# Kernel optimization log

Hardware: AMD Instinct MI355X
Metric: run time of the kernel (lower is better)

The kernel has to match this reference:

```python
import jax, jax.numpy as jnp
import numpy as np

NUM_CLS = 81
N_ROI = 512
N_POS = 128
OUT = 7
SAMP = 2
SCALES = (0.25, 0.125, 0.0625, 0.03125)


def _roi_align(feat, rois, out, scale, samp=SAMP):
    # feat: [C,H,W]; rois: [N,4] (x1,y1,x2,y2) in image coords. torchvision-style
    # ROIAlign, aligned=False, avg pool over samp x samp bilinear samples per bin.
    C, H, W = feat.shape
    b = rois * scale
    x1, y1, x2, y2 = b[:, 0], b[:, 1], b[:, 2], b[:, 3]
    bw = jnp.maximum(x2 - x1, 1.0) / out
    bh = jnp.maximum(y2 - y1, 1.0) / out
    N = rois.shape[0]
    # sample offsets within a roi, in bin units: [out, samp]
    grid = jnp.arange(out, dtype=feat.dtype)[:, None] + (jnp.arange(samp, dtype=feat.dtype)[None, :] + 0.5) / samp
    px = x1[:, None, None] + grid[None] * bw[:, None, None]  # [N,out,samp]
    py = y1[:, None, None] + grid[None] * bh[:, None, None]
    # full sampling grid [N, out_y, out_x, samp_y, samp_x]
    PX = jnp.broadcast_to(px[:, None, :, None, :], (N, out, out, samp, samp))
    PY = jnp.broadcast_to(py[:, :, None, :, None], (N, out, out, samp, samp))
    valid = (PX > -1.0) & (PX < W) & (PY > -1.0) & (PY < H)
    x = jnp.clip(PX, 0.0, W - 1.0)
    y = jnp.clip(PY, 0.0, H - 1.0)
    x0f = jnp.floor(x)
    y0f = jnp.floor(y)
    lx = x - x0f
    ly = y - y0f
    x0 = x0f.astype(jnp.int32)
    y0 = y0f.astype(jnp.int32)
    x1i = jnp.minimum(x0 + 1, W - 1)
    y1i = jnp.minimum(y0 + 1, H - 1)
    def g(yi, xi):
        return feat[:, yi, xi]  # [C,N,out,out,samp,samp]
    v = (g(y0, x0) * (1 - ly) * (1 - lx) + g(y0, x1i) * (1 - ly) * lx
         + g(y1i, x0) * ly * (1 - lx) + g(y1i, x1i) * ly * lx)
    v = v * valid.astype(feat.dtype)
    pooled = v.mean(axis=(-1, -2))  # [C,N,out,out]
    return pooled.transpose(1, 0, 2, 3)  # [N,C,out,out]


def setup_inputs() -> dict:
    key = jax.random.key(0)
    ks = jax.random.split(key, 16)
    H_IMG, W_IMG = 800.0, 1024.0
    P2 = jax.random.normal(ks[0], (1, 256, 200, 256), jnp.float32)
    P3 = jax.random.normal(ks[1], (1, 256, 100, 128), jnp.float32)
    P4 = jax.random.normal(ks[2], (1, 256, 50, 64), jnp.float32)
    P5 = jax.random.normal(ks[3], (1, 256, 25, 32), jnp.float32)
    x1 = jax.random.uniform(ks[4], (N_ROI,)) * (W_IMG - 64.0)
    y1 = jax.random.uniform(ks[5], (N_ROI,)) * (H_IMG - 64.0)
    w = jax.random.uniform(ks[6], (N_ROI,), minval=16.0, maxval=512.0)
    h = jax.random.uniform(ks[7], (N_ROI,), minval=16.0, maxval=512.0)
    rois = jnp.stack([x1, y1, jnp.minimum(x1 + w, W_IMG - 1.0), jnp.minimum(y1 + h, H_IMG - 1.0)], axis=-1)
    label = jax.random.randint(ks[8], (N_ROI,), 0, NUM_CLS, dtype=jnp.int32)
    loc = jax.random.normal(ks[9], (N_POS, 4), jnp.float32) * 0.1
    s = 0.02
    return {
        'P2': P2, 'P3': P3, 'P4': P4, 'P5': P5,
        'rois': rois, 'label': label, 'loc': loc,
        'W1': jax.random.normal(ks[10], (256 * OUT * OUT, 1024), jnp.float32) * s,
        'b1': jnp.zeros((1024,), jnp.float32),
        'W2': jax.random.normal(ks[11], (1024, 1024), jnp.float32) * s,
        'b2': jnp.zeros((1024,), jnp.float32),
        'Wcls': jax.random.normal(ks[12], (1024, NUM_CLS), jnp.float32) * s,
        'bcls': jnp.zeros((NUM_CLS,), jnp.float32),
        'Wloc': jax.random.normal(ks[13], (1024, NUM_CLS * 4), jnp.float32) * s,
        'bloc': jnp.zeros((NUM_CLS * 4,), jnp.float32),
    }


def reference(P2, P3, P4, P5, rois, label, loc, W1, b1, W2, b2, Wcls, bcls, Wloc, bloc):
    feats = (P2[0], P3[0], P4[0], P5[0])
    # FPN level assignment: floor(4 + log2(sqrt(area)/224)).clamp(2,5) - 2
    area = (rois[:, 2] - rois[:, 0] + 1.0) * (rois[:, 3] - rois[:, 1] + 1.0)
    lvl = jnp.floor(4.0 + jnp.log(jnp.sqrt(area) / 224.0) / np.log(2.0))
    lvl = (jnp.clip(lvl, 2.0, 5.0) - 2.0).astype(jnp.int32)  # [N] in {0,1,2,3}
    onehot = jax.nn.one_hot(lvl, 4, dtype=rois.dtype)  # [N,4]
    # pool every roi at all 4 levels, select assigned level (same values as
    # the original per-level grouping + argsort re-ordering)
    pooled = jnp.stack([_roi_align(f, rois, OUT, s) for f, s in zip(feats, SCALES)])  # [4,N,C,7,7]
    x = jnp.einsum('lnchw,nl->nchw', pooled, onehot)
    # Fast head
    x = x.reshape(x.shape[0], -1)
    h = jax.nn.relu(x @ W1 + b1)
    h = jax.nn.relu(h @ W2 + b2)
    logits = h @ Wcls + bcls                    # [N, num_cls]
    locp = (h @ Wloc + bloc).reshape(-1, NUM_CLS, 4)
    # loss assembly
    logp = jax.nn.log_softmax(logits, axis=-1)
    cls_loss = -jnp.take_along_axis(logp, label[:, None], axis=1).mean()
    loc_train = locp[jnp.arange(N_POS), label[:N_POS]]  # class-indexed gather
    t = jnp.abs(loc_train - loc)
    sl1 = jnp.where(t < 1.0, 0.5 * t * t, t - 0.5)  # SmoothL1, sigma=1
    box_loss = sl1.sum() / float(N_ROI)
    return cls_loss + box_loss
```

## Files before the change

### kernel.cpp

```cpp
#include <hip/hip_runtime.h>
#include <hip/hip_bf16.h>
#include <math.h>

#define N_ROI 512
#define N_POS 128
#define NUM_CLS 81
#define KDIM 12544
#define HID 1024

typedef __bf16 bf16x8 __attribute__((ext_vector_type(8)));
typedef __bf16 bf16x4 __attribute__((ext_vector_type(4)));
typedef float f32x4 __attribute__((ext_vector_type(4)));

__device__ inline void gload16(const void* g, void* lds) {
  __builtin_amdgcn_global_load_lds(
      (const __attribute__((address_space(1))) void*)g,
      (__attribute__((address_space(3))) void*)lds, 16, 0, 0);
}

__global__ __launch_bounds__(256) void roi_align_kernel(
    const float* __restrict__ P2, const float* __restrict__ P3,
    const float* __restrict__ P4, const float* __restrict__ P5,
    const float* __restrict__ rois, __bf16* __restrict__ xout) {
  int n = blockIdx.x;
  int t = threadIdx.x;

  __shared__ int    gxo[14];
  __shared__ float2 gxf[14];
  __shared__ int2   gyi[14];
  __shared__ float2 gyf[14];
  __shared__ int    s_lvl, s_HWb;

  float rx1 = rois[n * 4 + 0], ry1 = rois[n * 4 + 1];
  float rx2 = rois[n * 4 + 2], ry2 = rois[n * 4 + 3];
  float area = (rx2 - rx1 + 1.0f) * (ry2 - ry1 + 1.0f);
  float lf = floorf(4.0f + log2f(sqrtf(area) / 224.0f));
  lf = fminf(fmaxf(lf, 2.0f), 5.0f);
  int lvl = (int)lf - 2;

  const float scales[4] = {0.25f, 0.125f, 0.0625f, 0.03125f};
  const int   Hs[4] = {200, 100, 50, 25};
  const int   Ws[4] = {256, 128, 64, 32};
  float sc = scales[lvl];
  int H = Hs[lvl], W = Ws[lvl];

  float bx1 = rx1 * sc, by1 = ry1 * sc;
  float bw = fmaxf(rx2 * sc - bx1, 1.0f) * (1.0f / 7.0f);
  float bh = fmaxf(ry2 * sc - by1, 1.0f) * (1.0f / 7.0f);

  if (t < 14) {
    int i = t >> 1, j = t & 1;
    float g = (float)i + 0.25f + 0.5f * (float)j;
    float px = bx1 + g * bw;
    float vx = (px > -1.0f && px < (float)W) ? 1.0f : 0.0f;
    float xx = fminf(fmaxf(px, 0.0f), (float)(W - 1));
    float x0f = floorf(xx);
    int x0 = (int)x0f;
    int xa = min(x0, W - 2);
    float lxp = (x0 > xa) ? 1.0f : (xx - x0f);
    gxo[t] = xa * 4;
    gxf[t] = make_float2(lxp, vx);
    if (t == 0) { s_lvl = lvl; s_HWb = H * W * 4; }
  } else if (t >= 64 && t < 78) {
    int s = t - 64;
    int i = s >> 1, j = s & 1;
    float g = (float)i + 0.25f + 0.5f * (float)j;
    float py = by1 + g * bh;
    float vy = (py > -1.0f && py < (float)H) ? 1.0f : 0.0f;
    float yy = fminf(fmaxf(py, 0.0f), (float)(H - 1));
    float y0f = floorf(yy);
    int y0 = (int)y0f;
    int y1 = min(y0 + 1, H - 1);
    gyi[s] = make_int2(y0 * W * 4, y1 * W * 4);
    gyf[s] = make_float2(yy - y0f, vy);
  }
  __syncthreads();

  int lvl_s = __builtin_amdgcn_readfirstlane(s_lvl);
  const char* base = (const char*)(lvl_s == 0 ? P2 : lvl_s == 1 ? P3
                                   : lvl_s == 2 ? P4 : P5);
  int HWb = s_HWb;

  int wave = t >> 6, lane = t & 63;
  if (lane >= 49) return;

  int oh = (lane * 37) >> 8;
  int ow = lane - oh * 7;

  int2   xo = *(const int2*)&gxo[2 * ow];
  float4 xf = *(const float4*)&gxf[2 * ow];
  int4   yi = *(const int4*)&gyi[2 * oh];
  float4 yf = *(const float4*)&gyf[2 * oh];

  int off[8];
  off[0] = yi.x + xo.x; off[1] = yi.y + xo.x;
  off[2] = yi.x + xo.y; off[3] = yi.y + xo.y;
  off[4] = yi.z + xo.x; off[5] = yi.w + xo.x;
  off[6] = yi.z + xo.y; off[7] = yi.w + xo.y;

  float w00 = yf.y * xf.y, w01 = yf.y * xf.w;
  float w10 = yf.w * xf.y, w11 = yf.w * xf.w;

  int c0 = blockIdx.y * 16 + wave * 4;
  const char* bc0 = base + (size_t)c0 * HWb;

  float2 g[4][8];
#pragma unroll
  for (int ch = 0; ch < 4; ++ch) {
    const char* bcc = bc0 + (size_t)ch * HWb;
#pragma unroll
    for (int l = 0; l < 8; ++l)
      g[ch][l] = *(const float2*)(bcc + off[l]);
  }

  __bf16* outp = xout + (size_t)n * KDIM + (size_t)c0 * 49 + lane;
#pragma unroll
  for (int ch = 0; ch < 4; ++ch) {
    float s = 0.0f;
    {
      float fa = g[ch][0].x + xf.x * (g[ch][0].y - g[ch][0].x);
      float fb = g[ch][1].x + xf.x * (g[ch][1].y - g[ch][1].x);
      s += (fa + yf.x * (fb - fa)) * w00;
    }
    {
      float fa = g[ch][2].x + xf.z * (g[ch][2].y - g[ch][2].x);
      float fb = g[ch][3].x + xf.z * (g[ch][3].y - g[ch][3].x);
      s += (fa + yf.x * (fb - fa)) * w01;
    }
    {
      float fa = g[ch][4].x + xf.x * (g[ch][4].y - g[ch][4].x);
      float fb = g[ch][5].x + xf.x * (g[ch][5].y - g[ch][5].x);
      s += (fa + yf.z * (fb - fa)) * w10;
    }
    {
      float fa = g[ch][6].x + xf.z * (g[ch][6].y - g[ch][6].x);
      float fb = g[ch][7].x + xf.z * (g[ch][7].y - g[ch][7].x);
      s += (fa + yf.z * (fb - fa)) * w11;
    }
    outp[ch * 49] = (__bf16)(s * 0.25f);
  }
}

__global__ __launch_bounds__(256) void transpose_to_bf16_64(
    const float* __restrict__ src, __bf16* __restrict__ dst, int R, int C) {
  __shared__ float tile[64][65];
  int t = threadIdx.x;
  int bc = blockIdx.x * 64, br = blockIdx.y * 64;
  int rr = t >> 4, c4 = (t & 15) * 4;
#pragma unroll
  for (int p = 0; p < 4; ++p) {
    int r = p * 16 + rr;
    f32x4 v = *(const f32x4*)&src[(size_t)(br + r) * C + bc + c4];
    tile[r][c4] = v.x; tile[r][c4 + 1] = v.y;
    tile[r][c4 + 2] = v.z; tile[r][c4 + 3] = v.w;
  }
  __syncthreads();
#pragma unroll
  for (int p = 0; p < 2; ++p) {
    int group = t + 256 * p;
    int c = group >> 3;
    int r0 = (group & 7) * 8;
    bf16x8 o;
#pragma unroll
    for (int j = 0; j < 8; ++j) o[j] = (__bf16)tile[r0 + j][c];
    *(bf16x8*)&dst[(size_t)(bc + c) * R + br + r0] = o;
  }
}

__global__ __launch_bounds__(256) void transpose_pad_cls(
    const float* __restrict__ Wcls, __bf16* __restrict__ WcT) {
  __shared__ float tile[64][65];
  int t = threadIdx.x;
  int bk = blockIdx.x * 64;
  int bj = blockIdx.y * 64;
  int rr = t >> 4, c4 = (t & 15) * 4;
#pragma unroll
  for (int p = 0; p < 4; ++p) {
    int k = bk + p * 16 + rr;
#pragma unroll
    for (int i = 0; i < 4; ++i) {
      int j = bj + c4 + i;
      tile[p * 16 + rr][c4 + i] =
          (j < NUM_CLS) ? Wcls[(size_t)k * NUM_CLS + j] : 0.0f;
    }
  }
  __syncthreads();
#pragma unroll
  for (int p = 0; p < 4; ++p) {
    int c = p * 16 + rr;
    int r4 = c4;
    bf16x4 o = {(__bf16)tile[r4][c], (__bf16)tile[r4 + 1][c],
                (__bf16)tile[r4 + 2][c], (__bf16)tile[r4 + 3][c]};
    *(bf16x4*)&WcT[(size_t)(bj + c) * 1024 + bk + r4] = o;
  }
}

__global__ __launch_bounds__(256, 2) void mfma_gemm128(
    const __bf16* __restrict__ A, const __bf16* __restrict__ Bt,
    float* __restrict__ part, int M, int N, int K, int chunk) {
  __shared__ __align__(16) unsigned char smem[16384];
  unsigned char* As = smem;
  unsigned char* Bs = smem + 8192;

  int t = threadIdx.x;
  int wave = t >> 6;
  int lane = t & 63;
  int fr = lane & 15, q = lane >> 4;
  int bm = blockIdx.y * 128, bn = blockIdx.x * 128;
  int wm = (wave >> 1) * 64, wn = (wave & 1) * 64;

  int kbeg = blockIdx.z * chunk;
  int kend = min(K, kbeg + chunk);

  int qsrc = ((t & 3) - ((t >> 3) & 3)) & 3;
  const __bf16* a0 = A + (size_t)(bm + (t >> 2)) * K + kbeg + qsrc * 8;
  const __bf16* a1 = a0 + (size_t)64 * K;
  const __bf16* b0 = Bt + (size_t)(bn + (t >> 2)) * K + kbeg + qsrc * 8;
  const __bf16* b1 = b0 + (size_t)64 * K;
  unsigned char* AsW = As + wave * 1024;
  unsigned char* BsW = Bs + wave * 1024;

  int sA = ((q + (fr >> 1)) & 3) * 16;

  f32x4 acc[4][4];
#pragma unroll
  for (int i = 0; i < 4; ++i)
#pragma unroll
    for (int j = 0; j < 4; ++j) acc[i][j] = (f32x4){0.f, 0.f, 0.f, 0.f};

  for (int k0 = kbeg; k0 < kend; k0 += 32) {
    __syncthreads();
    gload16(a0, AsW);
    gload16(a1, AsW + 4096);
    gload16(b0, BsW);
    gload16(b1, BsW + 4096);
    a0 += 32; a1 += 32; b0 += 32; b1 += 32;
    __syncthreads();

    bf16x8 af[4], bfr[4];
#pragma unroll
    for (int i = 0; i < 4; ++i)
      af[i] = *(const bf16x8*)(As + (wm + 16 * i + fr) * 64 + sA);
#pragma unroll
    for (int j = 0; j < 4; ++j)
      bfr[j] = *(const bf16x8*)(Bs + (wn + 16 * j + fr) * 64 + sA);
#pragma unroll
    for (int i = 0; i < 4; ++i)
#pragma unroll
      for (int j = 0; j < 4; ++j)
        acc[i][j] = __builtin_amdgcn_mfma_f32_16x16x32_bf16(af[i], bfr[j],
                                                            acc[i][j], 0, 0, 0);
  }

  float* P = part + (size_t)blockIdx.z * M * N;
#pragma unroll
  for (int i = 0; i < 4; ++i) {
#pragma unroll
    for (int j = 0; j < 4; ++j) {
      int row0 = bm + wm + 16 * i + q * 4;
      int col = bn + wn + 16 * j + fr;
#pragma unroll
      for (int r = 0; r < 4; ++r)
        P[(size_t)(row0 + r) * N + col] = acc[i][j][r];
    }
  }
}

__global__ __launch_bounds__(256) void reduce_kernel(
    const float* __restrict__ part, int S, int MN, int Nmask,
    const float* __restrict__ bias, int bias_n, int relu,
    float* __restrict__ outf, __bf16* __restrict__ outb) {
  int i4 = (blockIdx.x * 256 + threadIdx.x) * 4;
  if (i4 >= MN) return;
  f32x4 s = {0.f, 0.f, 0.f, 0.f};
  for (int z = 0; z < S; ++z) {
    f32x4 v = *(const f32x4*)&part[(size_t)z * MN + i4];
    s.x += v.x; s.y += v.y; s.z += v.z; s.w += v.w;
  }
  int col = i4 & Nmask;
  float r[4] = {s.x, s.y, s.z, s.w};
#pragma unroll
  for (int j = 0; j < 4; ++j) {
    float b = (col + j < bias_n) ? bias[col + j] : 0.0f;
    float v = r[j] + b;
    if (relu) v = fmaxf(v, 0.0f);
    r[j] = v;
  }
  if (outf) {
    f32x4 o = {r[0], r[1], r[2], r[3]};
    *(f32x4*)&outf[i4] = o;
  }
  if (outb) {
    bf16x4 o = {(__bf16)r[0], (__bf16)r[1], (__bf16)r[2], (__bf16)r[3]};
    *(bf16x4*)&outb[i4] = o;
  }
}

__global__ __launch_bounds__(256) void loc_head_kernel(
    const float* __restrict__ h2, const float* __restrict__ Wloc,
    const float* __restrict__ bloc, const int* __restrict__ label,
    float* __restrict__ loct) {
  int n = blockIdx.x;
  int d = threadIdx.x >> 6;
  int lane = threadIdx.x & 63;
  int lab = label[n];
  const float* h = h2 + (size_t)n * HID;
  const float* w = Wloc + (size_t)lab * 4 + d;
  float s = 0.0f;
#pragma unroll
  for (int i = 0; i < 16; ++i) {
    int k = lane + i * 64;
    s += h[k] * w[(size_t)k * (NUM_CLS * 4)];
  }
#pragma unroll
  for (int off = 32; off > 0; off >>= 1) s += __shfl_down(s, off);
  if (lane == 0) loct[n * 4 + d] = s + bloc[lab * 4 + d];
}

__global__ __launch_bounds__(512) void loss_kernel(
    const float* __restrict__ logits, const int* __restrict__ label,
    const float* __restrict__ loct, const float* __restrict__ loc,
    float* __restrict__ out) {
  int t = threadIdx.x;
  const float* row = logits + (size_t)t * 128;
  float m = -1e30f;
  for (int j = 0; j < NUM_CLS; ++j) m = fmaxf(m, row[j]);
  float se = 0.0f;
  for (int j = 0; j < NUM_CLS; ++j) se += expf(row[j] - m);
  float cl = (m + logf(se)) - row[label[t]];

  float a = fabsf(loct[t] - loc[t]);
  float bl = (a < 1.0f) ? 0.5f * a * a : a - 0.5f;

  float v = cl + bl;
#pragma unroll
  for (int off = 32; off > 0; off >>= 1) v += __shfl_down(v, off);

  __shared__ float red[8];
  if ((t & 63) == 0) red[t >> 6] = v;
  __syncthreads();
  if (t == 0) {
    float tot = 0.0f;
    for (int i = 0; i < 8; ++i) tot += red[i];
    out[0] = tot * (1.0f / (float)N_ROI);
  }
}

extern "C" void kernel_launch(void* const* d_in, const int* in_sizes, int n_in,
                              void* d_out, int out_size, void* d_ws, size_t ws_size,
                              hipStream_t stream) {
  const float* P2   = (const float*)d_in[0];
  const float* P3   = (const float*)d_in[1];
  const float* P4   = (const float*)d_in[2];
  const float* P5   = (const float*)d_in[3];
  const float* rois = (const float*)d_in[4];
  const int*   label= (const int*)d_in[5];
  const float* loc  = (const float*)d_in[6];
  const float* W1   = (const float*)d_in[7];
  const float* b1   = (const float*)d_in[8];
  const float* W2   = (const float*)d_in[9];
  const float* b2   = (const float*)d_in[10];
  const float* Wcls = (const float*)d_in[11];
  const float* bcls = (const float*)d_in[12];
  const float* Wloc = (const float*)d_in[13];
  const float* bloc = (const float*)d_in[14];
  float* out = (float*)d_out;

  char* w = (char*)d_ws;
  __bf16* xb  = (__bf16*)w;  w += (size_t)N_ROI * KDIM * 2;
  __bf16* W1t = (__bf16*)w;  w += (size_t)KDIM * HID * 2;
  __bf16* W2t = (__bf16*)w;  w += (size_t)HID * HID * 2;
  __bf16* WcT = (__bf16*)w;  w += (size_t)128 * HID * 2;
  __bf16* h1b = (__bf16*)w;  w += (size_t)N_ROI * HID * 2;
  __bf16* h2b = (__bf16*)w;  w += (size_t)N_ROI * HID * 2;
  float*  h2f = (float*)w;   w += (size_t)N_ROI * HID * 4;
  float*  logits = (float*)w; w += (size_t)N_ROI * 128 * 4;
  float*  loct = (float*)w;  w += (size_t)N_ROI * 4;
  float*  part = (float*)w;

  transpose_to_bf16_64<<<dim3(HID / 64, KDIM / 64), 256, 0, stream>>>(W1, W1t,
                                                                      KDIM, HID);
  transpose_to_bf16_64<<<dim3(HID / 64, HID / 64), 256, 0, stream>>>(W2, W2t,
                                                                     HID, HID);
  transpose_pad_cls<<<dim3(16, 2), 256, 0, stream>>>(Wcls, WcT);
  roi_align_kernel<<<dim3(N_ROI, 16), 256, 0, stream>>>(P2, P3, P4, P5, rois,
                                                        xb);

  mfma_gemm128<<<dim3(HID / 128, N_ROI / 128, 16), 256, 0, stream>>>(
      xb, W1t, part, N_ROI, HID, KDIM, 800);
  reduce_kernel<<<(N_ROI * HID) / 1024, 256, 0, stream>>>(
      part, 16, N_ROI * HID, HID - 1, b1, HID, 1, nullptr, h1b);

  mfma_gemm128<<<dim3(HID / 128, N_ROI / 128, 8), 256, 0, stream>>>(
      h1b, W2t, part, N_ROI, HID, HID, 128);
  reduce_kernel<<<(N_ROI * HID) / 1024, 256, 0, stream>>>(
      part, 8, N_ROI * HID, HID - 1, b2, HID, 1, h2f, h2b);

  mfma_gemm128<<<dim3(1, N_ROI / 128, 4), 256, 0, stream>>>(
      h2b, WcT, part, N_ROI, 128, HID, 256);
  reduce_kernel<<<(N_ROI * 128) / 1024, 256, 0, stream>>>(
      part, 4, N_ROI * 128, 127, bcls, NUM_CLS, 0, logits, nullptr);

  loc_head_kernel<<<N_POS, 256, 0, stream>>>(h2f, Wloc, bloc, label, loct);
  loss_kernel<<<1, 512, 0, stream>>>(logits, label, loct, loc, out);
}
```

Baseline: 292.7 us.

## Fuse ROI-align and weight transposes into one prep kernel launch

Merges the ROI-align kernel and the three weight-transpose/convert kernels into a single launch that dispatches on block index, so independent work shares one grid and runs concurrently instead of as serial launches. Each ROI-align block now handles 8 channels per wave instead of 4, which raises register use. The class-head GEMM's split-K is doubled from 4 to 8, with a matching change to the reduce. The trade-off is higher register pressure in the fused kernel, tile shared memory that ROI blocks do not need, and more partial sums to reduce.

Result: faster. 284.9 us (-2.6%).

```diff
diff --git a/kernel.cpp b/kernel.cpp
--- a/kernel.cpp
+++ b/kernel.cpp
@@ -18,141 +18,168 @@
       (__attribute__((address_space(3))) void*)lds, 16, 0, 0);
 }
 
-__global__ __launch_bounds__(256) void roi_align_kernel(
+__global__ __launch_bounds__(256, 2) void prep_kernel(
     const float* __restrict__ P2, const float* __restrict__ P3,
     const float* __restrict__ P4, const float* __restrict__ P5,
-    const float* __restrict__ rois, __bf16* __restrict__ xout) {
-  int n = blockIdx.x;
-  int t = threadIdx.x;
-
+    const float* __restrict__ rois, __bf16* __restrict__ xout,
+    const float* __restrict__ W1, __bf16* __restrict__ W1t,
+    const float* __restrict__ W2, __bf16* __restrict__ W2t,
+    const float* __restrict__ Wcls, __bf16* __restrict__ WcT) {
+  __shared__ float tile[64][65];
   __shared__ int    gxo[14];
   __shared__ float2 gxf[14];
   __shared__ int2   gyi[14];
   __shared__ float2 gyf[14];
   __shared__ int    s_lvl, s_HWb;
 
-  float rx1 = rois[n * 4 + 0], ry1 = rois[n * 4 + 1];
-  float rx2 = rois[n * 4 + 2], ry2 = rois[n * 4 + 3];
-  float area = (rx2 - rx1 + 1.0f) * (ry2 - ry1 + 1.0f);
-  float lf = floorf(4.0f + log2f(sqrtf(area) / 224.0f));
-  lf = fminf(fmaxf(lf, 2.0f), 5.0f);
-  int lvl = (int)lf - 2;
-
-  const float scales[4] = {0.25f, 0.125f, 0.0625f, 0.03125f};
-  const int   Hs[4] = {200, 100, 50, 25};
-  const int   Ws[4] = {256, 128, 64, 32};
-  float sc = scales[lvl];
-  int H = Hs[lvl], W = Ws[lvl];
-
-  float bx1 = rx1 * sc, by1 = ry1 * sc;
-  float bw = fmaxf(rx2 * sc - bx1, 1.0f) * (1.0f / 7.0f);
-  float bh = fmaxf(ry2 * sc - by1, 1.0f) * (1.0f / 7.0f);
-
-  if (t < 14) {
-    int i = t >> 1, j = t & 1;
-    float g = (float)i + 0.25f + 0.5f * (float)j;
-    float px = bx1 + g * bw;
-    float vx = (px > -1.0f && px < (float)W) ? 1.0f : 0.0f;
-    float xx = fminf(fmaxf(px, 0.0f), (float)(W - 1));
-    float x0f = floorf(xx);
-    int x0 = (int)x0f;
-    int xa = min(x0, W - 2);
-    float lxp = (x0 > xa) ? 1.0f : (xx - x0f);
-    gxo[t] = xa * 4;
-    gxf[t] = make_float2(lxp, vx);
-    if (t == 0) { s_lvl = lvl; s_HWb = H * W * 4; }
-  } else if (t >= 64 && t < 78) {
-    int s = t - 64;
-    int i = s >> 1, j = s & 1;
-    float g = (float)i + 0.25f + 0.5f * (float)j;
-    float py = by1 + g * bh;
-    float vy = (py > -1.0f && py < (float)H) ? 1.0f : 0.0f;
-    float yy = fminf(fmaxf(py, 0.0f), (float)(H - 1));
-    float y0f = floorf(yy);
-    int y0 = (int)y0f;
-    int y1 = min(y0 + 1, H - 1);
-    gyi[s] = make_int2(y0 * W * 4, y1 * W * 4);
-    gyf[s] = make_float2(yy - y0f, vy);
-  }
-  __syncthreads();
-
-  int lvl_s = __builtin_amdgcn_readfirstlane(s_lvl);
-  const char* base = (const char*)(lvl_s == 0 ? P2 : lvl_s == 1 ? P3
-                                   : lvl_s == 2 ? P4 : P5);
-  int HWb = s_HWb;
-
-  int wave = t >> 6, lane = t & 63;
-  if (lane >= 49) return;
-
-  int oh = (lane * 37) >> 8;
-  int ow = lane - oh * 7;
-
-  int2   xo = *(const int2*)&gxo[2 * ow];
-  float4 xf = *(const float4*)&gxf[2 * ow];
-  int4   yi = *(const int4*)&gyi[2 * oh];
-  float4 yf = *(const float4*)&gyf[2 * oh];
-
-  int off[8];
-  off[0] = yi.x + xo.x; off[1] = yi.y + xo.x;
-  off[2] = yi.x + xo.y; off[3] = yi.y + xo.y;
-  off[4] = yi.z + xo.x; off[5] = yi.w + xo.x;
-  off[6] = yi.z + xo.y; off[7] = yi.w + xo.y;
-
-  float w00 = yf.y * xf.y, w01 = yf.y * xf.w;
-  float w10 = yf.w * xf.y, w11 = yf.w * xf.w;
-
-  int c0 = blockIdx.y * 16 + wave * 4;
-  const char* bc0 = base + (size_t)c0 * HWb;
-
-  float2 g[4][8];
-#pragma unroll
-  for (int ch = 0; ch < 4; ++ch) {
-    const char* bcc = bc0 + (size_t)ch * HWb;
-#pragma unroll
-    for (int l = 0; l < 8; ++l)
-      g[ch][l] = *(const float2*)(bcc + off[l]);
-  }
-
-  __bf16* outp = xout + (size_t)n * KDIM + (size_t)c0 * 49 + lane;
-#pragma unroll
-  for (int ch = 0; ch < 4; ++ch) {
-    float s = 0.0f;
-    {
-      float fa = g[ch][0].x + xf.x * (g[ch][0].y - g[ch][0].x);
-      float fb = g[ch][1].x + xf.x * (g[ch][1].y - g[ch][1].x);
+  int bid = blockIdx.x;
+  int t = threadIdx.x;
+
+  if (bid < 4096) {
+    int n = bid & 511;
+    int grp = bid >> 9;
+
+    float rx1 = rois[n * 4 + 0], ry1 = rois[n * 4 + 1];
+    float rx2 = rois[n * 4 + 2], ry2 = rois[n * 4 + 3];
+    float area = (rx2 - rx1 + 1.0f) * (ry2 - ry1 + 1.0f);
+    float lf = floorf(4.0f + log2f(sqrtf(area) / 224.0f));
+    lf = fminf(fmaxf(lf, 2.0f), 5.0f);
+    int lvl = (int)lf - 2;
+
+    const float scales[4] = {0.25f, 0.125f, 0.0625f, 0.03125f};
+    const int   Hs[4] = {200, 100, 50, 25};
+    const int   Ws[4] = {256, 128, 64, 32};
+    float sc = scales[lvl];
+    int H = Hs[lvl], W = Ws[lvl];
+
+    float bx1 = rx1 * sc, by1 = ry1 * sc;
+    float bw = fmaxf(rx2 * sc - bx1, 1.0f) * (1.0f / 7.0f);
+    float bh = fmaxf(ry2 * sc - by1, 1.0f) * (1.0f / 7.0f);
+
+    if (t < 14) {
+      int i = t >> 1, j = t & 1;
+      float g = (float)i + 0.25f + 0.5f * (float)j;
+      float px = bx1 + g * bw;
+      float vx = (px > -1.0f && px < (float)W) ? 1.0f : 0.0f;
+      float xx = fminf(fmaxf(px, 0.0f), (float)(W - 1));
+      float x0f = floorf(xx);
+      int x0 = (int)x0f;
+      int xa = min(x0, W - 2);
+      gxo[t] = xa * 4;
+      gxf[t] = make_float2((x0 > xa) ? 1.0f : (xx - x0f), vx);
+      if (t == 0) { s_lvl = lvl; s_HWb = H * W * 4; }
+    } else if (t >= 64 && t < 78) {
+      int s = t - 64;
+      int i = s >> 1, j = s & 1;
+      float g = (float)i + 0.25f + 0.5f * (float)j;
+      float py = by1 + g * bh;
+      float vy = (py > -1.0f && py < (float)H) ? 1.0f : 0.0f;
+      float yy = fminf(fmaxf(py, 0.0f), (float)(H - 1));
+      float y0f = floorf(yy);
+      int y0 = (int)y0f;
+      int y1 = min(y0 + 1, H - 1);
+      gyi[s] = make_int2(y0 * W * 4, y1 * W * 4);
+      gyf[s] = make_float2(yy - y0f, vy);
+    }
+    __syncthreads();
+
+    int lvl_s = __builtin_amdgcn_readfirstlane(s_lvl);
+    const char* base = (const char*)(lvl_s == 0 ? P2 : lvl_s == 1 ? P3
+                                     : lvl_s == 2 ? P4 : P5);
+    int HWb = s_HWb;
+
+    int wave = t >> 6, lane = t & 63;
+    if (lane >= 49) return;
+
+    int oh = (lane * 37) >> 8;
+    int ow = lane - oh * 7;
+
+    int2   xo = *(const int2*)&gxo[2 * ow];
+    float4 xf = *(const float4*)&gxf[2 * ow];
+    int4   yi = *(const int4*)&gyi[2 * oh];
+    float4 yf = *(const float4*)&gyf[2 * oh];
+
+    int off[8];
+    off[0] = yi.x + xo.x; off[1] = yi.y + xo.x;
+    off[2] = yi.x + xo.y; off[3] = yi.y + xo.y;
+    off[4] = yi.z + xo.x; off[5] = yi.w + xo.x;
+    off[6] = yi.z + xo.y; off[7] = yi.w + xo.y;
+
+    float w00 = yf.y * xf.y, w01 = yf.y * xf.w;
+    float w10 = yf.w * xf.y, w11 = yf.w * xf.w;
+
+    int c0 = grp * 32 + wave * 8;
+    const char* bc0 = base + (size_t)c0 * HWb;
+
+    float2 g[8][8];
+#pragma unroll
+    for (int ch = 0; ch < 8; ++ch) {
+      const char* bcc = bc0 + (size_t)ch * HWb;
+#pragma unroll
+      for (int l = 0; l < 8; ++l)
+        g[ch][l] = *(const float2*)(bcc + off[l]);
+    }
+
+    __bf16* outp = xout + (size_t)n * KDIM + (size_t)c0 * 49 + lane;
+#pragma unroll
+    for (int ch = 0; ch < 8; ++ch) {
+      float fa, fb, s = 0.0f;
+      fa = g[ch][0].x + xf.x * (g[ch][0].y - g[ch][0].x);
+      fb = g[ch][1].x + xf.x * (g[ch][1].y - g[ch][1].x);
       s += (fa + yf.x * (fb - fa)) * w00;
-    }
-    {
-      float fa = g[ch][2].x + xf.z * (g[ch][2].y - g[ch][2].x);
-      float fb = g[ch][3].x + xf.z * (g[ch][3].y - g[ch][3].x);
+      fa = g[ch][2].x + xf.z * (g[ch][2].y - g[ch][2].x);
+      fb = g[ch][3].x + xf.z * (g[ch][3].y - g[ch][3].x);
       s += (fa + yf.x * (fb - fa)) * w01;
-    }
-    {
-      float fa = g[ch][4].x + xf.x * (g[ch][4].y - g[ch][4].x);
-      float fb = g[ch][5].x + xf.x * (g[ch][5].y - g[ch][5].x);
+      fa = g[ch][4].x + xf.x * (g[ch][4].y - g[ch][4].x);
+      fb = g[ch][5].x + xf.x * (g[ch][5].y - g[ch][5].x);
       s += (fa + yf.z * (fb - fa)) * w10;
-    }
-    {
-      float fa = g[ch][6].x + xf.z * (g[ch][6].y - g[ch][6].x);
-      float fb = g[ch][7].x + xf.z * (g[ch][7].y - g[ch][7].x);
+      fa = g[ch][6].x + xf.z * (g[ch][6].y - g[ch][6].x);
+      fb = g[ch][7].x + xf.z * (g[ch][7].y - g[ch][7].x);
       s += (fa + yf.z * (fb - fa)) * w11;
-    }
-    outp[ch * 49] = (__bf16)(s * 0.25f);
-  }
-}
-
-__global__ __launch_bounds__(256) void transpose_to_bf16_64(
-    const float* __restrict__ src, __bf16* __restrict__ dst, int R, int C) {
-  __shared__ float tile[64][65];
-  int t = threadIdx.x;
-  int bc = blockIdx.x * 64, br = blockIdx.y * 64;
+      outp[ch * 49] = (__bf16)(s * 0.25f);
+    }
+    return;
+  }
+
+  const float* src;
+  __bf16* dst;
+  int R, C, bcb, brb;
+  bool pad_cls = false;
+  if (bid < 4096 + 3136) {
+    int id = bid - 4096;
+    src = W1; dst = W1t; R = KDIM; C = HID;
+    bcb = (id & 15) * 64; brb = (id >> 4) * 64;
+  } else if (bid < 4096 + 3136 + 256) {
+    int id = bid - (4096 + 3136);
+    src = W2; dst = W2t; R = HID; C = HID;
+    bcb = (id & 15) * 64; brb = (id >> 4) * 64;
+  } else {
+    int id = bid - (4096 + 3136 + 256);
+    src = Wcls; dst = WcT; R = HID; C = 128;
+    bcb = (id >> 4) * 64; brb = (id & 15) * 64;
+    pad_cls = true;
+  }
+
   int rr = t >> 4, c4 = (t & 15) * 4;
-#pragma unroll
-  for (int p = 0; p < 4; ++p) {
-    int r = p * 16 + rr;
-    f32x4 v = *(const f32x4*)&src[(size_t)(br + r) * C + bc + c4];
-    tile[r][c4] = v.x; tile[r][c4 + 1] = v.y;
-    tile[r][c4 + 2] = v.z; tile[r][c4 + 3] = v.w;
+  if (!pad_cls) {
+#pragma unroll
+    for (int p = 0; p < 4; ++p) {
+      int r = p * 16 + rr;
+      f32x4 v = *(const f32x4*)&src[(size_t)(brb + r) * C + bcb + c4];
+      tile[r][c4] = v.x; tile[r][c4 + 1] = v.y;
+      tile[r][c4 + 2] = v.z; tile[r][c4 + 3] = v.w;
+    }
+  } else {
+#pragma unroll
+    for (int p = 0; p < 4; ++p) {
+      int r = p * 16 + rr;
+#pragma unroll
+      for (int i = 0; i < 4; ++i) {
+        int j = bcb + c4 + i;
+        tile[r][c4 + i] =
+            (j < NUM_CLS) ? src[(size_t)(brb + r) * NUM_CLS + j] : 0.0f;
+      }
+    }
   }
   __syncthreads();
 #pragma unroll
@@ -163,35 +190,7 @@
     bf16x8 o;
 #pragma unroll
     for (int j = 0; j < 8; ++j) o[j] = (__bf16)tile[r0 + j][c];
-    *(bf16x8*)&dst[(size_t)(bc + c) * R + br + r0] = o;
-  }
-}
-
-__global__ __launch_bounds__(256) void transpose_pad_cls(
-    const float* __restrict__ Wcls, __bf16* __restrict__ WcT) {
-  __shared__ float tile[64][65];
-  int t = threadIdx.x;
-  int bk = blockIdx.x * 64;
-  int bj = blockIdx.y * 64;
-  int rr = t >> 4, c4 = (t & 15) * 4;
-#pragma unroll
-  for (int p = 0; p < 4; ++p) {
-    int k = bk + p * 16 + rr;
-#pragma unroll
-    for (int i = 0; i < 4; ++i) {
-      int j = bj + c4 + i;
-      tile[p * 16 + rr][c4 + i] =
-          (j < NUM_CLS) ? Wcls[(size_t)k * NUM_CLS + j] : 0.0f;
-    }
-  }
-  __syncthreads();
-#pragma unroll
-  for (int p = 0; p < 4; ++p) {
-    int c = p * 16 + rr;
-    int r4 = c4;
-    bf16x4 o = {(__bf16)tile[r4][c], (__bf16)tile[r4 + 1][c],
-                (__bf16)tile[r4 + 2][c], (__bf16)tile[r4 + 3][c]};
-    *(bf16x4*)&WcT[(size_t)(bj + c) * 1024 + bk + r4] = o;
+    *(bf16x8*)&dst[(size_t)(bcb + c) * R + brb + r0] = o;
   }
 }
 
@@ -378,13 +377,8 @@
   float*  loct = (float*)w;  w += (size_t)N_ROI * 4;
   float*  part = (float*)w;
 
-  transpose_to_bf16_64<<<dim3(HID / 64, KDIM / 64), 256, 0, stream>>>(W1, W1t,
-                                                                      KDIM, HID);
-  transpose_to_bf16_64<<<dim3(HID / 64, HID / 64), 256, 0, stream>>>(W2, W2t,
-                                                                     HID, HID);
-  transpose_pad_cls<<<dim3(16, 2), 256, 0, stream>>>(Wcls, WcT);
-  roi_align_kernel<<<dim3(N_ROI, 16), 256, 0, stream>>>(P2, P3, P4, P5, rois,
-                                                        xb);
+  prep_kernel<<<4096 + 3136 + 256 + 32, 256, 0, stream>>>(
+      P2, P3, P4, P5, rois, xb, W1, W1t, W2, W2t, Wcls, WcT);
 
   mfma_gemm128<<<dim3(HID / 128, N_ROI / 128, 16), 256, 0, stream>>>(
       xb, W1t, part, N_ROI, HID, KDIM, 800);
@@ -396,10 +390,10 @@
   reduce_kernel<<<(N_ROI * HID) / 1024, 256, 0, stream>>>(
       part, 8, N_ROI * HID, HID - 1, b2, HID, 1, h2f, h2b);
 
-  mfma_gemm128<<<dim3(1, N_ROI / 128, 4), 256, 0, stream>>>(
-      h2b, WcT, part, N_ROI, 128, HID, 256);
+  mfma_gemm128<<<dim3(1, N_ROI / 128, 8), 256, 0, stream>>>(
+      h2b, WcT, part, N_ROI, 128, HID, 128);
   reduce_kernel<<<(N_ROI * 128) / 1024, 256, 0, stream>>>(
-      part, 4, N_ROI * 128, 127, bcls, NUM_CLS, 0, logits, nullptr);
+      part, 8, N_ROI * 128, 127, bcls, NUM_CLS, 0, logits, nullptr);
 
   loc_head_kernel<<<N_POS, 256, 0, stream>>>(h2f, Wloc, bloc, label, loct);
   loss_kernel<<<1, 512, 0, stream>>>(logits, label, loct, loc, out);
```
